# Optimization experiments

Hardware: AMD Instinct MI355X
Metric: run time of the kernel (lower is better)

## Reference

```python
import jax, jax.numpy as jnp
import numpy as np

D_MODEL = 1024
NHEAD = 16
HEAD_DIM = D_MODEL // NHEAD
D_FF = 4096
EPS = 1e-5


def _linear(x, w, b):
    # torch Linear: y = x @ W^T + b, W is [out, in]
    return x @ w.T + b


def _layernorm(x, g, b):
    mu = jnp.mean(x, axis=-1, keepdims=True)
    var = jnp.var(x, axis=-1, keepdims=True)
    return (x - mu) * jax.lax.rsqrt(var + EPS) * g + b


def setup_inputs() -> dict:
    key = jax.random.key(0)
    ks = jax.random.split(key, 16)
    s = 0.02
    inp = {
        'x': jax.random.normal(ks[0], (2048, D_MODEL), jnp.float32),
        'q_in_w': s * jax.random.normal(ks[1], (D_MODEL, D_MODEL), jnp.float32),
        'q_in_b': jnp.zeros((D_MODEL,), jnp.float32),
        'k_in_w': s * jax.random.normal(ks[2], (D_MODEL, D_MODEL), jnp.float32),
        'k_in_b': jnp.zeros((D_MODEL,), jnp.float32),
        'v_in_w': s * jax.random.normal(ks[3], (D_MODEL, D_MODEL), jnp.float32),
        'v_in_b': jnp.zeros((D_MODEL,), jnp.float32),
        'out_w': s * jax.random.normal(ks[4], (D_MODEL, D_MODEL), jnp.float32),
        'out_b': jnp.zeros((D_MODEL,), jnp.float32),
        'ffn1_w': s * jax.random.normal(ks[5], (D_FF, D_MODEL), jnp.float32),
        'ffn1_b': jnp.zeros((D_FF,), jnp.float32),
        'ffn2_w': s * jax.random.normal(ks[6], (D_MODEL, D_FF), jnp.float32),
        'ffn2_b': jnp.zeros((D_MODEL,), jnp.float32),
        'n1_g': jnp.ones((D_MODEL,), jnp.float32),
        'n1_b': jnp.zeros((D_MODEL,), jnp.float32),
        'n2_g': jnp.ones((D_MODEL,), jnp.float32),
        'n2_b': jnp.zeros((D_MODEL,), jnp.float32),
        'q_out_w': s * jax.random.normal(ks[7], (D_MODEL, D_MODEL), jnp.float32),
        'q_out_b': jnp.zeros((D_MODEL,), jnp.float32),
        'k_out_w': s * jax.random.normal(ks[8], (D_MODEL, D_MODEL), jnp.float32),
        'k_out_b': jnp.zeros((D_MODEL,), jnp.float32),
        'v_out_w': s * jax.random.normal(ks[9], (D_MODEL, D_MODEL), jnp.float32),
        'v_out_b': jnp.zeros((D_MODEL,), jnp.float32),
        'seq_length': 2048,
    }
    return inp


def reference(x, q_in_w, q_in_b, k_in_w, k_in_b, v_in_w, v_in_b,
              out_w, out_b, ffn1_w, ffn1_b, ffn2_w, ffn2_b,
              n1_g, n1_b, n2_g, n2_b,
              q_out_w, q_out_b, k_out_w, k_out_b, v_out_w, v_out_b,
              seq_length):
    S = seq_length
    # --- is_first: batched in-projections (replaces per-token loop + cat) ---
    q_buf = _linear(x, q_in_w, q_in_b)   # [S, D]
    k_buf = _linear(x, k_in_w, k_in_b)
    v_buf = _linear(x, v_in_w, v_in_b)
    prev_layer_input = x

    # --- multi-head attention (non-causal, no mask) ---
    q = q_buf.reshape(S, NHEAD, HEAD_DIM).transpose(1, 0, 2)  # [H, S, Dh]
    k = k_buf.reshape(S, NHEAD, HEAD_DIM).transpose(1, 0, 2)
    v = v_buf.reshape(S, NHEAD, HEAD_DIM).transpose(1, 0, 2)
    scale = 1.0 / np.sqrt(HEAD_DIM).astype(np.float32)
    scores = jnp.einsum('hqd,hkd->hqk', q, k) * scale        # [H, S, S]
    attn = jax.nn.softmax(scores, axis=-1)
    ctx = jnp.einsum('hqk,hkd->hqd', attn, v)                # [H, S, Dh]
    attn_output = ctx.transpose(1, 0, 2).reshape(S, D_MODEL)  # [S, D]

    # --- post-norm residual blocks (batched over tokens) ---
    h = _linear(attn_output, out_w, out_b)
    h = _layernorm(prev_layer_input + h, n1_g, n1_b)
    ff = _linear(jax.nn.relu(_linear(h, ffn1_w, ffn1_b)), ffn2_w, ffn2_b)
    y = _layernorm(h + ff, n2_g, n2_b)                        # [S, D]

    # --- not is_last: out-projections for the next layer ---
    q_next = _linear(y, q_out_w, q_out_b)
    k_next = _linear(y, k_out_w, k_out_b)
    v_next = _linear(y, v_out_w, v_out_b)
    return (q_next, k_next, v_next, y)
```

## Files before the change

### kernel.cpp

```cpp
#include <hip/hip_runtime.h>
#include <math.h>

#define SEQ   2048
#define DM    1024
#define NH    16
#define DH    64
#define DFF   4096
#define KVSPLIT 4

typedef __bf16 bf16;
using bf16x8 = __attribute__((ext_vector_type(8))) __bf16;
using f32x4  = __attribute__((ext_vector_type(4))) float;

__device__ __forceinline__ unsigned short f2bfu(float f) {
    unsigned int u = __float_as_uint(f);
    u += 0x7FFF + ((u >> 16) & 1);
    return (unsigned short)(u >> 16);
}
__device__ __forceinline__ bf16 f2bf(float f) {
    unsigned short s = f2bfu(f);
    return __builtin_bit_cast(bf16, s);
}

__device__ __forceinline__ unsigned cvt_pk_bf16(float lo, float hi) {
    unsigned r;
    asm("v_cvt_pk_bf16_f32 %0, %1, %2" : "=v"(r) : "v"(lo), "v"(hi));
    return r;
}

__device__ __forceinline__ void gll16(const bf16* g, bf16* lds_base) {
    __builtin_amdgcn_global_load_lds(
        (const __attribute__((address_space(1))) unsigned int*)g,
        (__attribute__((address_space(3))) unsigned int*)lds_base, 16, 0, 0);
}

__global__ __launch_bounds__(256) void conv_k(const float* __restrict__ src,
                                              bf16* __restrict__ dst, int n) {
    int i = (blockIdx.x * 256 + threadIdx.x) * 4;
    if (i >= n) return;
    float4 v = *(const float4*)(src + i);
    ushort4 o;
    o.x = f2bfu(v.x); o.y = f2bfu(v.y); o.z = f2bfu(v.z); o.w = f2bfu(v.w);
    *(ushort4*)((unsigned short*)dst + i) = o;
}

struct ConvSeg  { const float* src; bf16* dst; int n; };
struct ConvSegs { ConvSeg s[6]; };

__global__ __launch_bounds__(256) void conv_multi_k(ConvSegs cs) {
    ConvSeg sg = cs.s[blockIdx.y];
    int i = (blockIdx.x * 256 + threadIdx.x) * 4;
    if (i >= sg.n) return;
    float4 v = *(const float4*)(sg.src + i);
    ushort4 o;
    o.x = f2bfu(v.x); o.y = f2bfu(v.y); o.z = f2bfu(v.z); o.w = f2bfu(v.w);
    *(ushort4*)((unsigned short*)sg.dst + i) = o;
}

struct GemmPtrs {
    const bf16* W[3];
    const float* bias[3];
    float* out32[3];
    bf16*  out16[3];
    float scale[3];
};

template<int BM, int BN, int BK>
__global__ __launch_bounds__(256) void gemm_bf16_k(
    const bf16* __restrict__ A, GemmPtrs p, int N, int K, int relu)
{
    constexpr int TM = BM / 32;
    constexpr int TN = BN / 32;
    constexpr int KK = BK / 32;
    constexpr int CH = BK / 8;
    __shared__ bf16 As[BM][BK];
    __shared__ bf16 Ws[BN][BK];

    const int t    = threadIdx.x;
    const int lane = t & 63;
    const int wave = t >> 6;
    const int quad = lane >> 4;
    const int l15  = lane & 15;
    const int wm   = (wave >> 1) * (BM / 2);
    const int wn   = (wave & 1) * (BN / 2);
    const int m0   = blockIdx.y * BM;
    const int n0   = blockIdx.x * BN;
    const int xm   = l15 & (CH - 1);
    const bf16* __restrict__ W = p.W[blockIdx.z];

    f32x4 acc[TM][TN];
    #pragma unroll
    for (int i = 0; i < TM; ++i)
        #pragma unroll
        for (int j = 0; j < TN; ++j)
            acc[i][j] = f32x4{0.f, 0.f, 0.f, 0.f};

    for (int k0 = 0; k0 < K; k0 += BK) {
        #pragma unroll
        for (int s = 0; s < BM * BK / 2048; ++s) {
            int base = s * 256 + wave * 64;
            int idx  = base + lane;
            int row  = idx / CH;
            int c    = idx % CH;
            gll16(A + (long)(m0 + row) * K + k0 + ((c ^ (row & (CH - 1))) * 8),
                  &As[0][0] + (long)base * 8);
        }
        #pragma unroll
        for (int s = 0; s < BN * BK / 2048; ++s) {
            int base = s * 256 + wave * 64;
            int idx  = base + lane;
            int row  = idx / CH;
            int c    = idx % CH;
            gll16(W + (long)(n0 + row) * K + k0 + ((c ^ (row & (CH - 1))) * 8),
                  &Ws[0][0] + (long)base * 8);
        }
        __syncthreads();

        bf16x8 a[TM][KK], b[TN][KK];
        #pragma unroll
        for (int i = 0; i < TM; ++i)
            #pragma unroll
            for (int kk = 0; kk < KK; ++kk)
                a[i][kk] = *(const bf16x8*)
                    &As[wm + i * 16 + l15][((kk * 4 + quad) ^ xm) * 8];
        #pragma unroll
        for (int j = 0; j < TN; ++j)
            #pragma unroll
            for (int kk = 0; kk < KK; ++kk)
                b[j][kk] = *(const bf16x8*)
                    &Ws[wn + j * 16 + l15][((kk * 4 + quad) ^ xm) * 8];
        #pragma unroll
        for (int kk = 0; kk < KK; ++kk)
            #pragma unroll
            for (int i = 0; i < TM; ++i)
                #pragma unroll
                for (int j = 0; j < TN; ++j)
                    acc[i][j] = __builtin_amdgcn_mfma_f32_16x16x32_bf16(
                        a[i][kk], b[j][kk], acc[i][j], 0, 0, 0);
        __syncthreads();
    }

    float* o32 = p.out32[blockIdx.z];
    bf16*  o16 = p.out16[blockIdx.z];
    const float* bias = p.bias[blockIdx.z];
    const float scl = p.scale[blockIdx.z];
    #pragma unroll
    for (int j = 0; j < TN; ++j) {
        int n = n0 + wn + j * 16 + l15;
        float bv = bias[n];
        #pragma unroll
        for (int i = 0; i < TM; ++i) {
            #pragma unroll
            for (int r = 0; r < 4; ++r) {
                int m = m0 + wm + i * 16 + quad * 4 + r;
                float v = (acc[i][j][r] + bv) * scl;
                if (relu) v = fmaxf(v, 0.f);
                if (o32) o32[(long)m * N + n] = v;
                if (o16) o16[(long)m * N + n] = f2bf(v);
            }
        }
    }
}

template<int BM, int BN, int BK, int KS>
__global__ __launch_bounds__(256) void gemm_splitk_k(
    const bf16* __restrict__ A, const bf16* __restrict__ W,
    float* __restrict__ part, int N, int K)
{
    constexpr int TM = BM / 32;
    constexpr int TN = BN / 32;
    constexpr int KK = BK / 32;
    constexpr int CH = BK / 8;
    __shared__ bf16 As[BM][BK];
    __shared__ bf16 Ws[BN][BK];

    const int t    = threadIdx.x;
    const int lane = t & 63;
    const int wave = t >> 6;
    const int quad = lane >> 4;
    const int l15  = lane & 15;
    const int wm   = (wave >> 1) * (BM / 2);
    const int wn   = (wave & 1) * (BN / 2);
    const int m0   = blockIdx.y * BM;
    const int n0   = blockIdx.x * BN;
    const int xm   = l15 & (CH - 1);
    const int Kp   = K / KS;
    const int klo  = blockIdx.z * Kp;
    const long MN  = (long)gridDim.y * BM * N;

    f32x4 acc[TM][TN];
    #pragma unroll
    for (int i = 0; i < TM; ++i)
        #pragma unroll
        for (int j = 0; j < TN; ++j)
            acc[i][j] = f32x4{0.f, 0.f, 0.f, 0.f};

    for (int k0 = klo; k0 < klo + Kp; k0 += BK) {
        #pragma unroll
        for (int s = 0; s < BM * BK / 2048; ++s) {
            int base = s * 256 + wave * 64;
            int idx  = base + lane;
            int row  = idx / CH;
            int c    = idx % CH;
            gll16(A + (long)(m0 + row) * K + k0 + ((c ^ (row & (CH - 1))) * 8),
                  &As[0][0] + (long)base * 8);
        }
        #pragma unroll
        for (int s = 0; s < BN * BK / 2048; ++s) {
            int base = s * 256 + wave * 64;
            int idx  = base + lane;
            int row  = idx / CH;
            int c    = idx % CH;
            gll16(W + (long)(n0 + row) * K + k0 + ((c ^ (row & (CH - 1))) * 8),
                  &Ws[0][0] + (long)base * 8);
        }
        __syncthreads();

        bf16x8 a[TM][KK], b[TN][KK];
        #pragma unroll
        for (int i = 0; i < TM; ++i)
            #pragma unroll
            for (int kk = 0; kk < KK; ++kk)
                a[i][kk] = *(const bf16x8*)
                    &As[wm + i * 16 + l15][((kk * 4 + quad) ^ xm) * 8];
        #pragma unroll
        for (int j = 0; j < TN; ++j)
            #pragma unroll
            for (int kk = 0; kk < KK; ++kk)
                b[j][kk] = *(const bf16x8*)
                    &Ws[wn + j * 16 + l15][((kk * 4 + quad) ^ xm) * 8];
        #pragma unroll
        for (int kk = 0; kk < KK; ++kk)
            #pragma unroll
            for (int i = 0; i < TM; ++i)
                #pragma unroll
                for (int j = 0; j < TN; ++j)
                    acc[i][j] = __builtin_amdgcn_mfma_f32_16x16x32_bf16(
                        a[i][kk], b[j][kk], acc[i][j], 0, 0, 0);
        __syncthreads();
    }

    float* o = part + (long)blockIdx.z * MN;
    #pragma unroll
    for (int j = 0; j < TN; ++j) {
        int n = n0 + wn + j * 16 + l15;
        #pragma unroll
        for (int i = 0; i < TM; ++i)
            #pragma unroll
            for (int r = 0; r < 4; ++r) {
                int m = m0 + wm + i * 16 + quad * 4 + r;
                o[(long)m * N + n] = acc[i][j][r];
            }
    }
}

__global__ __launch_bounds__(256) void attn_mfma_k(
    const bf16* __restrict__ Q, const bf16* __restrict__ Kg,
    const bf16* __restrict__ Vg, bf16* __restrict__ Opart,
    float* __restrict__ lpart)
{
    __shared__ bf16 Kb[64][64];
    __shared__ bf16 Vt[64][72];

    const int t    = threadIdx.x;
    const int lane = t & 63;
    const int wave = t >> 6;
    const int quad = lane >> 4;
    const int l15  = lane & 15;
    const int h    = blockIdx.y;
    const int q0   = blockIdx.x * 64;
    const int spl  = blockIdx.z;
    const int cb   = h * DH;
    const long SD  = (long)SEQ * DM;

    const int qrow = q0 + wave * 16 + l15;
    bf16x8 bQ[2];
    #pragma unroll
    for (int kh = 0; kh < 2; ++kh)
        bQ[kh] = *(const bf16x8*)(Q + (long)qrow * DM + cb + kh * 32 + quad * 8);

    f32x4 o_acc[4];
    #pragma unroll
    for (int dt = 0; dt < 4; ++dt) o_acc[dt] = f32x4{0.f, 0.f, 0.f, 0.f};
    float lsum = 0.f;

    const int kv_lo = spl * (SEQ / KVSPLIT);
    const int kv_hi = kv_lo + SEQ / KVSPLIT;

    for (int kv0 = kv_lo; kv0 < kv_hi; kv0 += 64) {
        __syncthreads();
        #pragma unroll
        for (int s = 0; s < 2; ++s) {
            int idx = s * 256 + t;
            int row = idx >> 3;
            int dg  = idx & 7;
            gll16(Kg + (long)(kv0 + row) * DM + cb + ((dg ^ (row & 7)) * 8),
                  &Kb[0][0] + (s * 256 + wave * 64) * 8);
        }
        #pragma unroll
        for (int s = 0; s < 2; ++s) {
            int idx = t + s * 256;
            int key = idx >> 3;
            int dg  = idx & 7;
            bf16x8 vv = *(const bf16x8*)(Vg + (long)(kv0 + key) * DM + cb + dg * 8);
            int vk  = (key & 0x20) | ((key & 0x0f) << 1) | ((key & 0x10) >> 4);
            int swz = vk ^ (dg * 8);
            #pragma unroll
            for (int j = 0; j < 8; ++j) Vt[dg * 8 + j][swz] = vv[j];
        }
        __syncthreads();

        float p[16];
        #pragma unroll
        for (int kt = 0; kt < 4; ++kt) {
            int krow = kt * 16 + l15;
            bf16x8 a0 = *(const bf16x8*)&Kb[krow][(quad ^ (l15 & 7)) * 8];
            bf16x8 a1 = *(const bf16x8*)&Kb[krow][((4 + quad) ^ (l15 & 7)) * 8];
            f32x4 sv = f32x4{0.f, 0.f, 0.f, 0.f};
            sv = __builtin_amdgcn_mfma_f32_16x16x32_bf16(a0, bQ[0], sv, 0, 0, 0);
            sv = __builtin_amdgcn_mfma_f32_16x16x32_bf16(a1, bQ[1], sv, 0, 0, 0);
            #pragma unroll
            for (int r = 0; r < 4; ++r) p[kt * 4 + r] = exp2f(sv[r]);
        }

        #pragma unroll
        for (int i = 0; i < 16; ++i) lsum += p[i];

        bf16x8 aP[2];
        #pragma unroll
        for (int c = 0; c < 2; ++c) {
            union { unsigned u[4]; bf16x8 v; } pk;
            #pragma unroll
            for (int w4 = 0; w4 < 4; ++w4)
                pk.u[w4] = cvt_pk_bf16(p[c * 8 + w4], p[c * 8 + 4 + w4]);
            aP[c] = pk.v;
        }

        #pragma unroll
        for (int dt = 0; dt < 4; ++dt) {
            int d   = dt * 16 + l15;
            int dgr = d >> 3;
            bf16x8 v0 = *(const bf16x8*)&Vt[d][(quad ^ dgr) * 8];
            bf16x8 v1 = *(const bf16x8*)&Vt[d][((4 + quad) ^ dgr) * 8];
            o_acc[dt] = __builtin_amdgcn_mfma_f32_16x16x32_bf16(aP[0], v0, o_acc[dt], 0, 0, 0);
            o_acc[dt] = __builtin_amdgcn_mfma_f32_16x16x32_bf16(aP[1], v1, o_acc[dt], 0, 0, 0);
        }
    }

    #pragma unroll
    for (int r = 0; r < 4; ++r) {
        int row = q0 + wave * 16 + quad * 4 + r;
        #pragma unroll
        for (int dt = 0; dt < 4; ++dt)
            Opart[(long)spl * SD + (long)row * DM + cb + dt * 16 + l15] =
                f2bf(o_acc[dt][r]);
    }
    lsum += __shfl_xor(lsum, 16);
    lsum += __shfl_xor(lsum, 32);
    if (quad == 0)
        lpart[((long)spl * NH + h) * SEQ + qrow] = lsum;
}

__global__ __launch_bounds__(256) void attn_reduce_k(
    const bf16* __restrict__ Opart, const float* __restrict__ lpart,
    bf16* __restrict__ O)
{
    const long SD = (long)SEQ * DM;
    long i = ((long)blockIdx.x * 256 + threadIdx.x) * 8;
    int row = (int)(i / DM);
    int h   = (int)((i % DM) / DH);

    float l = 0.f;
    #pragma unroll
    for (int k = 0; k < KVSPLIT; ++k)
        l += lpart[((long)k * NH + h) * SEQ + row];
    float inv = 1.f / l;

    float acc[8] = {};
    #pragma unroll
    for (int k = 0; k < KVSPLIT; ++k) {
        bf16x8 v = *(const bf16x8*)(Opart + (long)k * SD + i);
        #pragma unroll
        for (int j = 0; j < 8; ++j) acc[j] += (float)v[j];
    }
    bf16x8 o;
    #pragma unroll
    for (int j = 0; j < 8; ++j) o[j] = f2bf(acc[j] * inv);
    *(bf16x8*)(O + i) = o;
}

template<int NS>
__global__ __launch_bounds__(256) void ln_red_k(
    const float* __restrict__ part, const float* __restrict__ bias,
    const float* __restrict__ res, const float* __restrict__ g,
    const float* __restrict__ b, float* __restrict__ out32,
    bf16* __restrict__ out16)
{
    const long SD = (long)SEQ * DM;
    const int row = blockIdx.x;
    const int t   = threadIdx.x;
    const long off = (long)row * DM + (t << 2);

    float4 v = *(const float4*)(res + off);
    float4 bv0 = *(const float4*)(bias + (t << 2));
    v.x += bv0.x; v.y += bv0.y; v.z += bv0.z; v.w += bv0.w;
    #pragma unroll
    for (int z = 0; z < NS; ++z) {
        float4 pz = *(const float4*)(part + z * SD + off);
        v.x += pz.x; v.y += pz.y; v.z += pz.z; v.w += pz.w;
    }

    float s1 = v.x + v.y + v.z + v.w;
    float s2 = v.x * v.x + v.y * v.y + v.z * v.z + v.w * v.w;
    #pragma unroll
    for (int off2 = 32; off2 > 0; off2 >>= 1) {
        s1 += __shfl_xor(s1, off2);
        s2 += __shfl_xor(s2, off2);
    }
    __shared__ float red[8];
    int wid = t >> 6, lid = t & 63;
    if (lid == 0) { red[wid] = s1; red[4 + wid] = s2; }
    __syncthreads();
    s1 = red[0] + red[1] + red[2] + red[3];
    s2 = red[4] + red[5] + red[6] + red[7];

    float mu   = s1 * (1.f / DM);
    float var  = s2 * (1.f / DM) - mu * mu;
    float rstd = rsqrtf(var + 1e-5f);

    float4 gv = *(const float4*)(g + (t << 2));
    float4 bv = *(const float4*)(b + (t << 2));
    float4 ov;
    ov.x = (v.x - mu) * rstd * gv.x + bv.x;
    ov.y = (v.y - mu) * rstd * gv.y + bv.y;
    ov.z = (v.z - mu) * rstd * gv.z + bv.z;
    ov.w = (v.w - mu) * rstd * gv.w + bv.w;
    if (out32) *(float4*)(out32 + off) = ov;
    if (out16) {
        ushort4 o;
        o.x = f2bfu(ov.x); o.y = f2bfu(ov.y); o.z = f2bfu(ov.z); o.w = f2bfu(ov.w);
        *(ushort4*)((unsigned short*)out16 + off) = o;
    }
}

extern "C" void kernel_launch(void* const* d_in, const int* in_sizes, int n_in,
                              void* d_out, int out_size, void* d_ws, size_t ws_size,
                              hipStream_t stream)
{
    const float* x       = (const float*)d_in[0];
    const float* q_in_w  = (const float*)d_in[1];
    const float* q_in_b  = (const float*)d_in[2];
    const float* k_in_w  = (const float*)d_in[3];
    const float* k_in_b  = (const float*)d_in[4];
    const float* v_in_w  = (const float*)d_in[5];
    const float* v_in_b  = (const float*)d_in[6];
    const float* out_w   = (const float*)d_in[7];
    const float* out_b   = (const float*)d_in[8];
    const float* ffn1_w  = (const float*)d_in[9];
    const float* ffn1_b  = (const float*)d_in[10];
    const float* ffn2_w  = (const float*)d_in[11];
    const float* ffn2_b  = (const float*)d_in[12];
    const float* n1_g    = (const float*)d_in[13];
    const float* n1_b    = (const float*)d_in[14];
    const float* n2_g    = (const float*)d_in[15];
    const float* n2_b    = (const float*)d_in[16];
    const float* q_out_w = (const float*)d_in[17];
    const float* q_out_b = (const float*)d_in[18];
    const float* k_out_w = (const float*)d_in[19];
    const float* k_out_b = (const float*)d_in[20];
    const float* v_out_w = (const float*)d_in[21];
    const float* v_out_b = (const float*)d_in[22];

    float* out = (float*)d_out;
    const long SD = (long)SEQ * DM;
    const long MB = 1024 * 1024;

    char* w = (char*)d_ws;
    bf16*  xbf   = (bf16*)(w);
    float* lpart = (float*)(w);
    bf16*  qb    = (bf16*)(w + 4  * MB);
    bf16*  kb    = (bf16*)(w + 8  * MB);
    bf16*  vb    = (bf16*)(w + 12 * MB);
    bf16*  atnb  = (bf16*)(w + 16 * MB);
    float* h32   = (float*)(w);
    bf16*  h16   = (bf16*)(w + 8  * MB);
    float* P2    = (float*)(w + 8  * MB);
    bf16*  Opart = (bf16*)(w + 20 * MB);
    float* P1    = (float*)(w + 20 * MB);
    bf16*  f1    = (bf16*)(w + 24 * MB);
    bf16*  wqi   = (bf16*)(w + 32 * MB);
    bf16*  wki   = (bf16*)(w + 34 * MB);
    bf16*  wvi   = (bf16*)(w + 36 * MB);
    bf16*  wo    = (bf16*)(w + 38 * MB);
    bf16*  wf1   = (bf16*)(w + 40 * MB);
    bf16*  wf2   = (bf16*)(w + 40 * MB);
    bf16*  wqo   = (bf16*)(w + 24 * MB);
    bf16*  wko   = (bf16*)(w + 26 * MB);
    bf16*  wvo   = (bf16*)(w + 28 * MB);
    bf16*  ybf   = (bf16*)(w + 30 * MB);
    float* y32   = out + 3 * SD;

    dim3 blk(256);
    const int DD = DM * DM;
    const float SCL = 0.18033688f;

    {
        ConvSegs cs;
        cs.s[0] = {x,      xbf, (int)SD};
        cs.s[1] = {q_in_w, wqi, DD};
        cs.s[2] = {k_in_w, wki, DD};
        cs.s[3] = {v_in_w, wvi, DD};
        cs.s[4] = {out_w,  wo,  DD};
        cs.s[5] = {ffn1_w, wf1, DM * DFF};
        conv_multi_k<<<dim3(DM * DFF / 1024, 6), blk, 0, stream>>>(cs);
    }

    {
        GemmPtrs p{};
        p.W[0] = wqi; p.W[1] = wki; p.W[2] = wvi;
        p.bias[0] = q_in_b; p.bias[1] = k_in_b; p.bias[2] = v_in_b;
        p.out16[0] = qb; p.out16[1] = kb; p.out16[2] = vb;
        p.scale[0] = SCL; p.scale[1] = 1.0f; p.scale[2] = 1.0f;
        gemm_bf16_k<128, 64, 64><<<dim3(DM / 64, SEQ / 128, 3), blk, 0, stream>>>(
            xbf, p, DM, DM, 0);
    }

    attn_mfma_k<<<dim3(SEQ / 64, NH, KVSPLIT), blk, 0, stream>>>(
        qb, kb, vb, Opart, lpart);
    attn_reduce_k<<<dim3((int)(SD / 2048)), blk, 0, stream>>>(Opart, lpart, atnb);

    gemm_splitk_k<64, 128, 64, 2><<<dim3(DM / 128, SEQ / 64, 2), blk, 0, stream>>>(
        atnb, wo, P1, DM, DM);

    ln_red_k<2><<<SEQ, blk, 0, stream>>>(P1, out_b, x, n1_g, n1_b, h32, h16);

    {
        GemmPtrs p{};
        p.W[0] = wf1; p.bias[0] = ffn1_b; p.out16[0] = f1;
        p.scale[0] = 1.0f; p.scale[1] = 1.0f; p.scale[2] = 1.0f;
        gemm_bf16_k<128, 64, 64><<<dim3(DFF / 64, SEQ / 128, 1), blk, 0, stream>>>(
            h16, p, DFF, DM, 1);
    }

    conv_k<<<dim3(DM * DFF / 1024), blk, 0, stream>>>(ffn2_w, wf2, DM * DFF);

    gemm_splitk_k<64, 128, 64, 2><<<dim3(DM / 128, SEQ / 64, 2), blk, 0, stream>>>(
        f1, wf2, P2, DM, DFF);

    {
        ConvSegs cs;
        cs.s[0] = {q_out_w, wqo, DD};
        cs.s[1] = {k_out_w, wko, DD};
        cs.s[2] = {v_out_w, wvo, DD};
        cs.s[3] = cs.s[0]; cs.s[4] = cs.s[0]; cs.s[5] = cs.s[0];
        conv_multi_k<<<dim3(DD / 1024, 3), blk, 0, stream>>>(cs);
    }

    ln_red_k<2><<<SEQ, blk, 0, stream>>>(P2, ffn2_b, h32, n2_g, n2_b, y32, ybf);

    {
        GemmPtrs p{};
        p.W[0] = wqo; p.W[1] = wko; p.W[2] = wvo;
        p.bias[0] = q_out_b; p.bias[1] = k_out_b; p.bias[2] = v_out_b;
        p.out32[0] = out; p.out32[1] = out + SD; p.out32[2] = out + 2 * SD;
        p.scale[0] = 1.0f; p.scale[1] = 1.0f; p.scale[2] = 1.0f;
        gemm_bf16_k<128, 64, 64><<<dim3(DM / 64, SEQ / 128, 3), blk, 0, stream>>>(
            ybf, p, DM, DM, 0);
    }
}
```

Measured before the change: 325.4 us.

## Drop attention KV-split and reduce kernel; add XCD-aware block swizzle to kernels

```diff
diff --git a/kernel.cpp b/kernel.cpp
--- a/kernel.cpp
+++ b/kernel.cpp
@@ -6,7 +6,6 @@
 #define NH    16
 #define DH    64
 #define DFF   4096
-#define KVSPLIT 4
 
 typedef __bf16 bf16;
 using bf16x8 = __attribute__((ext_vector_type(8))) __bf16;
@@ -32,6 +31,10 @@
     __builtin_amdgcn_global_load_lds(
         (const __attribute__((address_space(1))) unsigned int*)g,
         (__attribute__((address_space(3))) unsigned int*)lds_base, 16, 0, 0);
+}
+
+__device__ __forceinline__ int xcd_swz(int wid, int nwg) {
+    return (wid & 7) * (nwg >> 3) + (wid >> 3);
 }
 
 __global__ __launch_bounds__(256) void conv_k(const float* __restrict__ src,
@@ -76,6 +79,14 @@
     __shared__ bf16 As[BM][BK];
     __shared__ bf16 Ws[BN][BK];
 
+    const int nwg = gridDim.x * gridDim.y * gridDim.z;
+    const int wid = blockIdx.x + gridDim.x * (blockIdx.y + gridDim.y * blockIdx.z);
+    const int sw  = xcd_swz(wid, nwg);
+    const int bx  = sw % gridDim.x;
+    const int rem = sw / gridDim.x;
+    const int by  = rem % gridDim.y;
+    const int bz  = rem / gridDim.y;
+
     const int t    = threadIdx.x;
     const int lane = t & 63;
     const int wave = t >> 6;
@@ -83,10 +94,10 @@
     const int l15  = lane & 15;
     const int wm   = (wave >> 1) * (BM / 2);
     const int wn   = (wave & 1) * (BN / 2);
-    const int m0   = blockIdx.y * BM;
-    const int n0   = blockIdx.x * BN;
+    const int m0   = by * BM;
+    const int n0   = bx * BN;
     const int xm   = l15 & (CH - 1);
-    const bf16* __restrict__ W = p.W[blockIdx.z];
+    const bf16* __restrict__ W = p.W[bz];
 
     f32x4 acc[TM][TN];
     #pragma unroll
@@ -140,10 +151,10 @@
         __syncthreads();
     }
 
-    float* o32 = p.out32[blockIdx.z];
-    bf16*  o16 = p.out16[blockIdx.z];
-    const float* bias = p.bias[blockIdx.z];
-    const float scl = p.scale[blockIdx.z];
+    float* o32 = p.out32[bz];
+    bf16*  o16 = p.out16[bz];
+    const float* bias = p.bias[bz];
+    const float scl = p.scale[bz];
     #pragma unroll
     for (int j = 0; j < TN; ++j) {
         int n = n0 + wn + j * 16 + l15;
@@ -174,6 +185,14 @@
     __shared__ bf16 As[BM][BK];
     __shared__ bf16 Ws[BN][BK];
 
+    const int nwg = gridDim.x * gridDim.y * gridDim.z;
+    const int wid = blockIdx.x + gridDim.x * (blockIdx.y + gridDim.y * blockIdx.z);
+    const int sw  = xcd_swz(wid, nwg);
+    const int bx  = sw % gridDim.x;
+    const int rem = sw / gridDim.x;
+    const int by  = rem % gridDim.y;
+    const int bz  = rem / gridDim.y;
+
     const int t    = threadIdx.x;
     const int lane = t & 63;
     const int wave = t >> 6;
@@ -181,11 +200,11 @@
     const int l15  = lane & 15;
     const int wm   = (wave >> 1) * (BM / 2);
     const int wn   = (wave & 1) * (BN / 2);
-    const int m0   = blockIdx.y * BM;
-    const int n0   = blockIdx.x * BN;
+    const int m0   = by * BM;
+    const int n0   = bx * BN;
     const int xm   = l15 & (CH - 1);
     const int Kp   = K / KS;
-    const int klo  = blockIdx.z * Kp;
+    const int klo  = bz * Kp;
     const long MN  = (long)gridDim.y * BM * N;
 
     f32x4 acc[TM][TN];
@@ -240,7 +259,7 @@
         __syncthreads();
     }
 
-    float* o = part + (long)blockIdx.z * MN;
+    float* o = part + (long)bz * MN;
     #pragma unroll
     for (int j = 0; j < TN; ++j) {
         int n = n0 + wn + j * 16 + l15;
@@ -256,22 +275,23 @@
 
 __global__ __launch_bounds__(256) void attn_mfma_k(
     const bf16* __restrict__ Q, const bf16* __restrict__ Kg,
-    const bf16* __restrict__ Vg, bf16* __restrict__ Opart,
-    float* __restrict__ lpart)
+    const bf16* __restrict__ Vg, bf16* __restrict__ O)
 {
     __shared__ bf16 Kb[64][64];
     __shared__ bf16 Vt[64][72];
+
+    const int nwg = gridDim.x * gridDim.y;
+    const int wid = blockIdx.x + gridDim.x * blockIdx.y;
+    const int sw  = xcd_swz(wid, nwg);
+    const int h   = sw / gridDim.x;
+    const int q0  = (sw % gridDim.x) * 64;
 
     const int t    = threadIdx.x;
     const int lane = t & 63;
     const int wave = t >> 6;
     const int quad = lane >> 4;
     const int l15  = lane & 15;
-    const int h    = blockIdx.y;
-    const int q0   = blockIdx.x * 64;
-    const int spl  = blockIdx.z;
     const int cb   = h * DH;
-    const long SD  = (long)SEQ * DM;
 
     const int qrow = q0 + wave * 16 + l15;
     bf16x8 bQ[2];
@@ -284,10 +304,7 @@
     for (int dt = 0; dt < 4; ++dt) o_acc[dt] = f32x4{0.f, 0.f, 0.f, 0.f};
     float lsum = 0.f;
 
-    const int kv_lo = spl * (SEQ / KVSPLIT);
-    const int kv_hi = kv_lo + SEQ / KVSPLIT;
-
-    for (int kv0 = kv_lo; kv0 < kv_hi; kv0 += 64) {
+    for (int kv0 = 0; kv0 < SEQ; kv0 += 64) {
         __syncthreads();
         #pragma unroll
         for (int s = 0; s < 2; ++s) {
@@ -347,46 +364,16 @@
         }
     }
 
-    #pragma unroll
-    for (int r = 0; r < 4; ++r) {
-        int row = q0 + wave * 16 + quad * 4 + r;
-        #pragma unroll
-        for (int dt = 0; dt < 4; ++dt)
-            Opart[(long)spl * SD + (long)row * DM + cb + dt * 16 + l15] =
-                f2bf(o_acc[dt][r]);
-    }
     lsum += __shfl_xor(lsum, 16);
     lsum += __shfl_xor(lsum, 32);
-    if (quad == 0)
-        lpart[((long)spl * NH + h) * SEQ + qrow] = lsum;
-}
-
-__global__ __launch_bounds__(256) void attn_reduce_k(
-    const bf16* __restrict__ Opart, const float* __restrict__ lpart,
-    bf16* __restrict__ O)
-{
-    const long SD = (long)SEQ * DM;
-    long i = ((long)blockIdx.x * 256 + threadIdx.x) * 8;
-    int row = (int)(i / DM);
-    int h   = (int)((i % DM) / DH);
-
-    float l = 0.f;
-    #pragma unroll
-    for (int k = 0; k < KVSPLIT; ++k)
-        l += lpart[((long)k * NH + h) * SEQ + row];
-    float inv = 1.f / l;
-
-    float acc[8] = {};
-    #pragma unroll
-    for (int k = 0; k < KVSPLIT; ++k) {
-        bf16x8 v = *(const bf16x8*)(Opart + (long)k * SD + i);
-        #pragma unroll
-        for (int j = 0; j < 8; ++j) acc[j] += (float)v[j];
-    }
-    bf16x8 o;
-    #pragma unroll
-    for (int j = 0; j < 8; ++j) o[j] = f2bf(acc[j] * inv);
-    *(bf16x8*)(O + i) = o;
+    #pragma unroll
+    for (int r = 0; r < 4; ++r) {
+        float inv = 1.f / __shfl(lsum, quad * 4 + r, 16);
+        int row = q0 + wave * 16 + quad * 4 + r;
+        #pragma unroll
+        for (int dt = 0; dt < 4; ++dt)
+            O[(long)row * DM + cb + dt * 16 + l15] = f2bf(o_acc[dt][r] * inv);
+    }
 }
 
 template<int NS>
@@ -477,7 +464,6 @@
 
     char* w = (char*)d_ws;
     bf16*  xbf   = (bf16*)(w);
-    float* lpart = (float*)(w);
     bf16*  qb    = (bf16*)(w + 4  * MB);
     bf16*  kb    = (bf16*)(w + 8  * MB);
     bf16*  vb    = (bf16*)(w + 12 * MB);
@@ -485,7 +471,6 @@
     float* h32   = (float*)(w);
     bf16*  h16   = (bf16*)(w + 8  * MB);
     float* P2    = (float*)(w + 8  * MB);
-    bf16*  Opart = (bf16*)(w + 20 * MB);
     float* P1    = (float*)(w + 20 * MB);
     bf16*  f1    = (bf16*)(w + 24 * MB);
     bf16*  wqi   = (bf16*)(w + 32 * MB);
@@ -525,9 +510,7 @@
             xbf, p, DM, DM, 0);
     }
 
-    attn_mfma_k<<<dim3(SEQ / 64, NH, KVSPLIT), blk, 0, stream>>>(
-        qb, kb, vb, Opart, lpart);
-    attn_reduce_k<<<dim3((int)(SD / 2048)), blk, 0, stream>>>(Opart, lpart, atnb);
+    attn_mfma_k<<<dim3(SEQ / 64, NH), blk, 0, stream>>>(qb, kb, vb, atnb);
 
     gemm_splitk_k<64, 128, 64, 2><<<dim3(DM / 128, SEQ / 64, 2), blk, 0, stream>>>(
         atnb, wo, P1, DM, DM);
```

Result: slower. 350.0 us (+7.5%).
